# Kernel optimization log

Measured on AMD Instinct MI355X. Metric: run time of the kernel, lower is better.

The kernel has to match this reference:

```python
import jax, jax.numpy as jnp
import numpy as np

H = 4  # num_heads

def _ln(x, g, b):
    m = x.mean(-1, keepdims=True)
    v = ((x - m) ** 2).mean(-1, keepdims=True)
    return (x - m) * jax.lax.rsqrt(v + 1e-5) * g + b

def _mlp(x, w1, b1, w2, b2):
    return jax.nn.relu(x @ w1 + b1) @ w2 + b2

def _lin_att(q, k, v):
    # q,k,v: [BB, L, H, hd] ; linear (kernelized) attention, no softmax
    L = q.shape[1]
    qn = q / jnp.maximum(jnp.linalg.norm(q, axis=-1, keepdims=True), 1e-12)
    kn = k / jnp.maximum(jnp.linalg.norm(k, axis=-1, keepdims=True), 1e-12)
    kvs = jnp.einsum('blhm,blhd->bhmd', kn, v)
    num = jnp.einsum('bnhm,bhmd->bnhd', qn, kvs) + L * v
    den = jnp.einsum('bnhm,bhm->bnh', qn, kn.sum(axis=1))[..., None] + L
    return num / den

def _fast_attn(x4, w_qkv, w_op, b_op):
    # x4: [B,T,N,D]; spatial attention over N, temporal attention over T, concat, project
    B, T, N, D = x4.shape
    hd = D // H
    q, k, v = jnp.split(x4 @ w_qkv, 3, axis=-1)
    sh = lambda t: t.reshape(B * T, N, H, hd)
    out_s = _lin_att(sh(q), sh(k), sh(v)).reshape(B, T, N, D)
    th = lambda t: jnp.swapaxes(t, 1, 2).reshape(B * N, T, H, hd)
    out_t = jnp.swapaxes(_lin_att(th(q), th(k), th(v)).reshape(B, N, T, D), 1, 2)
    return jnp.concatenate([out_s, out_t], axis=-1) @ w_op + b_op

def _forward(x, W_in, b_in, adp, W_tp, b_tp, qkv_w, op_w, op_b, pw_w, pw_b,
             fc_w1, fc_b1, fc_w2, fc_b2, ln1_g, ln1_b, ln2_g, ln2_b,
             ep_w, ep_b, enc_w1, enc_b1, enc_w2, enc_b2, out_w, out_b):
    Nn, T, _ = x.shape
    xt = jnp.swapaxes(x, 0, 1)[None]                 # [1,T,N,in]
    h = xt @ W_in + b_in                             # input_proj -> [1,T,N,24]
    h = jnp.concatenate([h, adp[None]], axis=-1)     # + adaptive emb -> [1,T,N,104]
    h = h @ W_tp + b_tp                              # temporal_proj: 1x1 conv == pointwise linear
    graph = jnp.einsum('tnd,tmd->tnm', adp, adp)     # [T,N,N]
    graph = jax.nn.softmax(jax.nn.relu(graph), axis=-1)  # AvgPool(1,1) is identity
    # GraphPropagate (order=2, eval/no-dropout): [h, graph @ h]
    z1 = jnp.einsum('tni,btid->btnd', graph, h)
    att0 = _fast_attn(h, qkv_w[0], op_w[0], op_b[0])
    att1 = _fast_attn(z1, qkv_w[1], op_w[1], op_b[1])
    # scale = [1, 0.01]; note torch's in-place aliasing makes ln1 input = 2*x_glo
    g = h + att0 * (h @ pw_w[0] + pw_b[0]) + 0.01 * att1 * (att0 @ pw_w[1] + pw_b[1])
    h1 = _ln(2.0 * g, ln1_g, ln1_b)
    h2 = _ln(h1 + _mlp(h1, fc_w1, fc_b1, fc_w2, fc_b2), ln2_g, ln2_b)
    y = jnp.swapaxes(h2, 1, 2).reshape(1, Nn, T * h2.shape[-1]) @ ep_w + ep_b  # encoder_proj
    for i in range(enc_w1.shape[0]):                 # 3 residual MLP blocks
        y = y + _mlp(y, enc_w1[i], enc_b1[i], enc_w2[i], enc_b2[i])
    out = y @ out_w + out_b                          # [1,N,365]
    return out.reshape(Nn, T, 1)

def setup_inputs() -> dict:
    key = jax.random.key(0)
    ks = jax.random.split(key, 24)
    f = lambda i, shape, s=0.05: jax.random.normal(ks[i], shape, dtype=jnp.float32) * s
    D, T, N, IN = 104, 365, 400, 3
    return {
        'x': jax.random.normal(ks[0], (N, T, IN), dtype=jnp.float32),
        'W_in': f(1, (IN, 24)), 'b_in': f(2, (24,)),
        'adp': f(3, (T, N, 80)),
        'W_tp': f(4, (D, D)), 'b_tp': f(5, (D,)),
        'qkv_w': f(6, (2, D, 3 * D)),
        'op_w': f(7, (2, 2 * D, D)), 'op_b': f(8, (2, D)),
        'pw_w': f(9, (2, D, D)), 'pw_b': f(10, (2, D)),
        'fc_w1': f(11, (D, 2 * D)), 'fc_b1': f(12, (2 * D,)),
        'fc_w2': f(13, (2 * D, D)), 'fc_b2': f(14, (D,)),
        'ln1_g': jnp.ones((D,), jnp.float32), 'ln1_b': jnp.zeros((D,), jnp.float32),
        'ln2_g': jnp.ones((D,), jnp.float32), 'ln2_b': jnp.zeros((D,), jnp.float32),
        'ep_w': f(15, (T * D, D), 0.01), 'ep_b': f(16, (D,)),
        'enc_w1': f(17, (3, D, 2 * D)), 'enc_b1': f(18, (3, 2 * D)),
        'enc_w2': f(19, (3, 2 * D, D)), 'enc_b2': f(20, (3, D)),
        'out_w': f(21, (D, T)), 'out_b': f(22, (T,)),
    }

def reference(x, W_in, b_in, adp, W_tp, b_tp, qkv_w, op_w, op_b, pw_w, pw_b,
              fc_w1, fc_b1, fc_w2, fc_b2, ln1_g, ln1_b, ln2_g, ln2_b,
              ep_w, ep_b, enc_w1, enc_b1, enc_w2, enc_b2, out_w, out_b):
    return _forward(x, W_in, b_in, adp, W_tp, b_tp, qkv_w, op_w, op_b, pw_w, pw_b,
                    fc_w1, fc_b1, fc_w2, fc_b2, ln1_g, ln1_b, ln2_g, ln2_b,
                    ep_w, ep_b, enc_w1, enc_b1, enc_w2, enc_b2, out_w, out_b)
```

## Files before the change

### kernel.cpp

```cpp
#include <hip/hip_runtime.h>
#include <hip/hip_bf16.h>
#include <cstddef>

#define TT   365
#define NN   400
#define TN   (TT*NN)
#define HD   26
#define NH   4

#define CEILDIV(a,b) (((a)+(b)-1)/(b))

typedef __hip_bfloat16 bf16;
typedef short short8v __attribute__((ext_vector_type(8)));
typedef float float4v __attribute__((ext_vector_type(4)));
typedef float float16v __attribute__((ext_vector_type(16)));
__device__ __forceinline__ float b2f(bf16 v){ return __bfloat162float(v); }
__device__ __forceinline__ bf16  f2b(float v){ return __float2bfloat16(v); }

static constexpr size_t NB0 = (size_t)TN*104;
static constexpr size_t NB1 = (size_t)TN*104;
static constexpr size_t NB2 = (size_t)TN*312;
static constexpr size_t NB3 = (size_t)TN*104;
static constexpr size_t NBF = NB0+NB1+NB2+NB3;
static constexpr size_t NTILE   = (size_t)108*32;
static constexpr size_t NKVSB_S = (size_t)TT*NTILE;
static constexpr size_t NKVSB_T = (size_t)NN*NTILE;
static constexpr size_t NY      = (size_t)NN*104;
static constexpr size_t NW_TP   = 104*128;
static constexpr size_t NW_QKV  = 312*128;
static constexpr size_t NW_OP   = 104*224;
static constexpr size_t NW_PW   = 104*128;
static constexpr size_t NW_FC1  = 208*128;
static constexpr size_t NW_FC2  = 104*224;
static constexpr size_t NW_EPT  = (size_t)104*37960;
static constexpr size_t NWT     = NW_TP + 2*NW_QKV + 2*NW_OP + 2*NW_PW + NW_FC1 + NW_FC2 + NW_EPT;
static constexpr size_t WS_NEEDED = NBF*2 + (NKVSB_S+NKVSB_T)*2 + NY*4 + NWT*2;
static constexpr size_t NADP_ROWS = (size_t)TN + 64;
static constexpr size_t NADP = NADP_ROWS*96;
static constexpr size_t NHT  = ((size_t)TT*104 + 8)*448;
static_assert(NADP + NHT <= NB2, "z1 scratch must fit in B2");

__global__ void __launch_bounds__(256) prep_w(
    const float* __restrict__ W, bf16* __restrict__ Wt, int K, int Nc, int KP)
{
    int idx = blockIdx.x*256 + threadIdx.x;
    if (idx >= Nc*KP) return;
    int n = idx / KP, k = idx - n*KP;
    Wt[idx] = (k < K) ? f2b(W[(size_t)k*Nc + n]) : f2b(0.f);
}

__global__ void __launch_bounds__(256) prep_wT(
    const float* __restrict__ W, bf16* __restrict__ Wt)
{
    __shared__ float T[64][105];
    int k0 = blockIdx.x * 64;
    int tid = threadIdx.x;
    for (int idx = tid; idx < 64*104; idx += 256) {
        int r = idx / 104, c = idx - r*104;
        int k = k0 + r;
        T[r][c] = (k < 37960) ? W[(size_t)k*104 + c] : 0.f;
    }
    __syncthreads();
    for (int idx = tid; idx < 104*32; idx += 256) {
        int n = idx >> 5, kp = idx & 31;
        int k = kp*2;
        if (k0 + k + 1 < 37960 || k0 + k < 37960) {
            if (k0 + k < 37960) {
                bf16 lo = f2b(T[k][n]);
                bf16 hi = f2b(T[k+1][n]);
                uint v = ((uint)(*(ushort*)&hi) << 16) | (*(ushort*)&lo);
                if (k0 + k + 1 < 37960) *(uint*)(Wt + (size_t)n*37960 + k0 + k) = v;
                else Wt[(size_t)n*37960 + k0 + k] = lo;
            }
        }
    }
}

__global__ void __launch_bounds__(256) prep_adp(
    const float* __restrict__ adp, bf16* __restrict__ out)
{
    size_t i = (size_t)blockIdx.x*256 + threadIdx.x;
    if (i >= NADP) return;
    size_t row = i / 96; int e = (int)(i - row*96);
    float v = (row < TN && e < 80) ? adp[row*80 + e] : 0.f;
    out[i] = f2b(v);
}

__global__ void __launch_bounds__(256) ht_kernel(
    const bf16* __restrict__ h, bf16* __restrict__ hT)
{
    __shared__ bf16 As[64*106];
    int t = blockIdx.y, n0 = blockIdx.x*64;
    int tid = threadIdx.x;
    for (int idx = tid; idx < 64*52; idx += 256) {
        int r = idx / 52, k = idx - r*52;
        int n = n0 + r;
        uint v = 0;
        if (n < NN) v = *(const uint*)(h + ((size_t)t*NN + n)*104 + k*2);
        *(uint*)(&As[r*106 + k*2]) = v;
    }
    __syncthreads();
    for (int idx = tid; idx < 104*32; idx += 256) {
        int d = idx >> 5, np = idx & 31;
        int n = np*2;
        ushort lo = *(ushort*)&As[n*106 + d];
        ushort hi = *(ushort*)&As[(n+1)*106 + d];
        uint v = ((uint)hi << 16) | lo;
        *(uint*)(hT + ((size_t)t*104 + d)*448 + n0 + n) = v;
    }
}

__global__ void __launch_bounds__(128) hcat_kernel(
    const float* __restrict__ x, const float* __restrict__ W_in,
    const float* __restrict__ b_in, const float* __restrict__ adp,
    bf16* __restrict__ hcat)
{
    int bid = blockIdx.x;
    int t = bid / NN, n = bid - t*NN;
    int tid = threadIdx.x;
    if (tid < 24) {
        float s = b_in[tid];
        size_t xb = ((size_t)n*TT + t)*3;
        #pragma unroll
        for (int i = 0; i < 3; ++i) s += x[xb + i] * W_in[i*24 + tid];
        hcat[(size_t)bid*104 + tid] = f2b(s);
    } else if (tid < 104) {
        hcat[(size_t)bid*104 + tid] = f2b(adp[(size_t)bid*80 + (tid - 24)]);
    }
}

template<int KP>
__global__ void __launch_bounds__(256) gemm_mf(
    const bf16* __restrict__ A, int lda, int K,
    const bf16* __restrict__ Wt, const float* __restrict__ bias,
    bf16* __restrict__ C, int M, int Nc, int relu)
{
    constexpr int STR = KP + 8;
    constexpr int KPQ = KP/8;
    __shared__ bf16 As[64*STR];
    __shared__ bf16 Ws[64*STR];
    int m0 = blockIdx.x * 64;
    int c0 = blockIdx.y * 64;
    int tid = threadIdx.x;
    const int KQ = K/8;
    uint4 z4 = {0u,0u,0u,0u};
    for (int idx = tid; idx < 64*KPQ; idx += 256) {
        int r = idx / KPQ, q = idx - r*KPQ;
        int m = m0 + r;
        uint4 v = z4;
        if (m < M && q < KQ) v = *(const uint4*)(A + (size_t)m*lda + q*8);
        *(uint4*)(&As[r*STR + q*8]) = v;
    }
    for (int idx = tid; idx < 64*KPQ; idx += 256) {
        int r = idx / KPQ, q = idx - r*KPQ;
        int n = c0 + r;
        uint4 v = z4;
        if (n < Nc) v = *(const uint4*)(Wt + (size_t)n*KP + q*8);
        *(uint4*)(&Ws[r*STR + q*8]) = v;
    }
    __syncthreads();

    int lane = tid & 63, w = tid >> 6;
    int n16 = lane & 15, quad = lane >> 4;
    constexpr int KS = KP/32;
    short8v af[KS];
    #pragma unroll
    for (int s = 0; s < KS; ++s)
        af[s] = *(const short8v*)(&As[(16*w + n16)*STR + s*32 + quad*8]);
    float4v acc[4];
    #pragma unroll
    for (int ct = 0; ct < 4; ++ct) { float4v z = {0.f,0.f,0.f,0.f}; acc[ct] = z; }
    #pragma unroll
    for (int ct = 0; ct < 4; ++ct) {
        #pragma unroll
        for (int s = 0; s < KS; ++s) {
            short8v bfr = *(const short8v*)(&Ws[(ct*16 + n16)*STR + s*32 + quad*8]);
            acc[ct] = __builtin_amdgcn_mfma_f32_16x16x32_bf16(af[s], bfr, acc[ct], 0, 0, 0);
        }
    }
    #pragma unroll
    for (int ct = 0; ct < 4; ++ct) {
        int c = c0 + ct*16 + n16;
        if (c < Nc) {
            float b = bias ? bias[c] : 0.f;
            #pragma unroll
            for (int reg = 0; reg < 4; ++reg) {
                int m = m0 + 16*w + quad*4 + reg;
                if (m < M) {
                    float v = acc[ct][reg] + b;
                    if (relu) v = fmaxf(v, 0.f);
                    C[(size_t)m*Nc + c] = f2b(v);
                }
            }
        }
    }
}

__global__ void __launch_bounds__(256) gate_ln1(
    bf16* __restrict__ h, const bf16* __restrict__ att0, const bf16* __restrict__ att1,
    const bf16* __restrict__ w0t, const bf16* __restrict__ w1t, const float* __restrict__ pwb,
    const float* __restrict__ gamma, const float* __restrict__ beta)
{
    constexpr int STR = 136;
    __shared__ bf16 A0s[64*STR];
    __shared__ bf16 A1s[64*STR];
    __shared__ bf16 Ws[112*STR];
    __shared__ float prm[416];
    int m0 = blockIdx.x * 64;
    int tid = threadIdx.x;
    int lane = tid & 63, w = tid >> 6, n16 = lane & 15, quad = lane >> 4;
    uint4 z4 = {0u,0u,0u,0u};

    for (int idx = tid; idx < 64*16; idx += 256) {
        int r = idx >> 4, q = idx & 15;
        int m = m0 + r;
        uint4 v0 = z4, v1 = z4;
        if (m < TN && q < 13) {
            v0 = *(const uint4*)(h    + (size_t)m*104 + q*8);
            v1 = *(const uint4*)(att0 + (size_t)m*104 + q*8);
        }
        *(uint4*)(&A0s[r*STR + q*8]) = v0;
        *(uint4*)(&A1s[r*STR + q*8]) = v1;
    }
    for (int idx = tid; idx < 112*16; idx += 256) {
        int c = idx >> 4, q = idx & 15;
        uint4 v = z4;
        if (c < 104) v = *(const uint4*)(w0t + (size_t)c*128 + q*8);
        *(uint4*)(&Ws[c*STR + q*8]) = v;
    }
    for (int i = tid; i < 416; i += 256)
        prm[i] = (i < 208) ? pwb[i] : (i < 312 ? gamma[i-208] : beta[i-312]);
    __syncthreads();

    short8v a0f[4], a1f[4];
    #pragma unroll
    for (int s = 0; s < 4; ++s) {
        a0f[s] = *(const short8v*)(&A0s[(16*w + n16)*STR + s*32 + quad*8]);
        a1f[s] = *(const short8v*)(&A1s[(16*w + n16)*STR + s*32 + quad*8]);
    }
    float4v acc0[7], acc1[7];
    #pragma unroll
    for (int ct = 0; ct < 7; ++ct) { float4v z = {0.f,0.f,0.f,0.f}; acc0[ct] = z; acc1[ct] = z; }
    #pragma unroll
    for (int ct = 0; ct < 7; ++ct)
        #pragma unroll
        for (int s = 0; s < 4; ++s) {
            short8v bfr = *(const short8v*)(&Ws[(ct*16 + n16)*STR + s*32 + quad*8]);
            acc0[ct] = __builtin_amdgcn_mfma_f32_16x16x32_bf16(a0f[s], bfr, acc0[ct], 0, 0, 0);
        }
    __syncthreads();
    for (int idx = tid; idx < 112*16; idx += 256) {
        int c = idx >> 4, q = idx & 15;
        uint4 v = z4;
        if (c < 104) v = *(const uint4*)(w1t + (size_t)c*128 + q*8);
        *(uint4*)(&Ws[c*STR + q*8]) = v;
    }
    __syncthreads();
    #pragma unroll
    for (int ct = 0; ct < 7; ++ct)
        #pragma unroll
        for (int s = 0; s < 4; ++s) {
            short8v bfr = *(const short8v*)(&Ws[(ct*16 + n16)*STR + s*32 + quad*8]);
            acc1[ct] = __builtin_amdgcn_mfma_f32_16x16x32_bf16(a1f[s], bfr, acc1[ct], 0, 0, 0);
        }

    float sum[4] = {0.f,0.f,0.f,0.f};
    #pragma unroll
    for (int ct = 0; ct < 7; ++ct) {
        int c = ct*16 + n16;
        bool colok = c < 104;
        float b0 = colok ? prm[c] : 0.f;
        float b1 = colok ? prm[104 + c] : 0.f;
        #pragma unroll
        for (int reg = 0; reg < 4; ++reg) {
            int r = 16*w + quad*4 + reg;
            int m = m0 + r;
            float xv = 0.f;
            if (colok && m < TN) {
                float p0 = acc0[ct][reg] + b0;
                float p1 = acc1[ct][reg] + b1;
                float hv = b2f(A0s[r*STR + c]);
                float a0 = b2f(A1s[r*STR + c]);
                float a1 = b2f(att1[(size_t)m*104 + c]);
                xv = 2.f*(hv + a0*p0 + 0.01f*a1*p1);
            }
            acc0[ct][reg] = xv;
            sum[reg] += xv;
        }
    }
    #pragma unroll
    for (int reg = 0; reg < 4; ++reg) {
        float v = sum[reg];
        v += __shfl_xor(v,1,64); v += __shfl_xor(v,2,64);
        v += __shfl_xor(v,4,64); v += __shfl_xor(v,8,64);
        sum[reg] = v * (1.f/104.f);
    }
    float var[4] = {0.f,0.f,0.f,0.f};
    #pragma unroll
    for (int ct = 0; ct < 7; ++ct) {
        bool colok = (ct*16 + n16) < 104;
        #pragma unroll
        for (int reg = 0; reg < 4; ++reg) {
            if (colok) {
                float d = acc0[ct][reg] - sum[reg];
                acc0[ct][reg] = d;
                var[reg] += d*d;
            }
        }
    }
    #pragma unroll
    for (int reg = 0; reg < 4; ++reg) {
        float v = var[reg];
        v += __shfl_xor(v,1,64); v += __shfl_xor(v,2,64);
        v += __shfl_xor(v,4,64); v += __shfl_xor(v,8,64);
        var[reg] = rsqrtf(v * (1.f/104.f) + 1e-5f);
    }
    #pragma unroll
    for (int ct = 0; ct < 7; ++ct) {
        int c = ct*16 + n16;
        if (c < 104) {
            float g = prm[208 + c], be = prm[312 + c];
            #pragma unroll
            for (int reg = 0; reg < 4; ++reg) {
                int m = m0 + 16*w + quad*4 + reg;
                if (m < TN)
                    h[(size_t)m*104 + c] = f2b(acc0[ct][reg]*var[reg]*g + be);
            }
        }
    }
}

__global__ void __launch_bounds__(256) fc2_ln2(
    const bf16* __restrict__ hidden, const bf16* __restrict__ w2t, const float* __restrict__ b2,
    const bf16* __restrict__ h1, const float* __restrict__ gamma, const float* __restrict__ beta,
    bf16* __restrict__ h2)
{
    constexpr int STRA = 232;
    constexpr int STRW = 136;
    __shared__ bf16 As[64*STRA];
    __shared__ bf16 Ws[112*STRW];
    __shared__ float prm[312];
    int m0 = blockIdx.x * 64;
    int tid = threadIdx.x;
    int lane = tid & 63, w = tid >> 6, n16 = lane & 15, quad = lane >> 4;
    uint4 z4 = {0u,0u,0u,0u};

    for (int idx = tid; idx < 64*28; idx += 256) {
        int r = idx / 28, q = idx - r*28;
        int m = m0 + r;
        uint4 v = z4;
        if (m < TN && q < 26) v = *(const uint4*)(hidden + (size_t)m*208 + q*8);
        *(uint4*)(&As[r*STRA + q*8]) = v;
    }
    for (int idx = tid; idx < 112*16; idx += 256) {
        int c = idx >> 4, q = idx & 15;
        uint4 v = z4;
        if (c < 104) v = *(const uint4*)(w2t + (size_t)c*224 + q*8);
        *(uint4*)(&Ws[c*STRW + q*8]) = v;
    }
    for (int i = tid; i < 312; i += 256)
        prm[i] = (i < 104) ? b2[i] : (i < 208 ? gamma[i-104] : beta[i-208]);
    __syncthreads();

    short8v af[7];
    #pragma unroll
    for (int s = 0; s < 7; ++s)
        af[s] = *(const short8v*)(&As[(16*w + n16)*STRA + s*32 + quad*8]);
    float4v acc[7];
    #pragma unroll
    for (int ct = 0; ct < 7; ++ct) { float4v z = {0.f,0.f,0.f,0.f}; acc[ct] = z; }
    #pragma unroll
    for (int ct = 0; ct < 7; ++ct)
        #pragma unroll
        for (int s = 0; s < 4; ++s) {
            short8v bfr = *(const short8v*)(&Ws[(ct*16 + n16)*STRW + s*32 + quad*8]);
            acc[ct] = __builtin_amdgcn_mfma_f32_16x16x32_bf16(af[s], bfr, acc[ct], 0, 0, 0);
        }
    __syncthreads();
    for (int idx = tid; idx < 112*16; idx += 256) {
        int c = idx >> 4, q = idx & 15;
        uint4 v = z4;
        if (c < 104 && q < 12) v = *(const uint4*)(w2t + (size_t)c*224 + 128 + q*8);
        *(uint4*)(&Ws[c*STRW + q*8]) = v;
    }
    __syncthreads();
    #pragma unroll
    for (int ct = 0; ct < 7; ++ct)
        #pragma unroll
        for (int s = 4; s < 7; ++s) {
            short8v bfr = *(const short8v*)(&Ws[(ct*16 + n16)*STRW + (s-4)*32 + quad*8]);
            acc[ct] = __builtin_amdgcn_mfma_f32_16x16x32_bf16(af[s], bfr, acc[ct], 0, 0, 0);
        }

    float sum[4] = {0.f,0.f,0.f,0.f};
    #pragma unroll
    for (int ct = 0; ct < 7; ++ct) {
        int c = ct*16 + n16;
        bool colok = c < 104;
        float bb = colok ? prm[c] : 0.f;
        #pragma unroll
        for (int reg = 0; reg < 4; ++reg) {
            int m = m0 + 16*w + quad*4 + reg;
            float xv = 0.f;
            if (colok && m < TN)
                xv = b2f(h1[(size_t)m*104 + c]) + acc[ct][reg] + bb;
            acc[ct][reg] = xv;
            sum[reg] += xv;
        }
    }
    #pragma unroll
    for (int reg = 0; reg < 4; ++reg) {
        float v = sum[reg];
        v += __shfl_xor(v,1,64); v += __shfl_xor(v,2,64);
        v += __shfl_xor(v,4,64); v += __shfl_xor(v,8,64);
        sum[reg] = v * (1.f/104.f);
    }
    float var[4] = {0.f,0.f,0.f,0.f};
    #pragma unroll
    for (int ct = 0; ct < 7; ++ct) {
        bool colok = (ct*16 + n16) < 104;
        #pragma unroll
        for (int reg = 0; reg < 4; ++reg) {
            if (colok) {
                float d = acc[ct][reg] - sum[reg];
                acc[ct][reg] = d;
                var[reg] += d*d;
            }
        }
    }
    #pragma unroll
    for (int reg = 0; reg < 4; ++reg) {
        float v = var[reg];
        v += __shfl_xor(v,1,64); v += __shfl_xor(v,2,64);
        v += __shfl_xor(v,4,64); v += __shfl_xor(v,8,64);
        var[reg] = rsqrtf(v * (1.f/104.f) + 1e-5f);
    }
    #pragma unroll
    for (int ct = 0; ct < 7; ++ct) {
        int c = ct*16 + n16;
        if (c < 104) {
            float g = prm[104 + c], be = prm[208 + c];
            #pragma unroll
            for (int reg = 0; reg < 4; ++reg) {
                int m = m0 + 16*w + quad*4 + reg;
                if (m < TN)
                    h2[(size_t)m*104 + c] = f2b(acc[ct][reg]*var[reg]*g + be);
            }
        }
    }
}

__global__ void __launch_bounds__(256) ep_mf(
    const bf16* __restrict__ h2, const bf16* __restrict__ wt, float* __restrict__ y)
{
    constexpr int STR = 136;
    __shared__ bf16 As[64*STR];
    __shared__ bf16 Ws[64*STR];
    int m0 = blockIdx.x * 64;
    int c0 = blockIdx.y * 64;
    int t0 = blockIdx.z * 8;
    int t1 = min(TT, t0 + 8);
    int tid = threadIdx.x;
    int lane = tid & 63, w = tid >> 6, n16 = lane & 15, quad = lane >> 4;
    uint4 z4 = {0u,0u,0u,0u};

    float4v acc[4];
    #pragma unroll
    for (int ct = 0; ct < 4; ++ct) { float4v z = {0.f,0.f,0.f,0.f}; acc[ct] = z; }

    for (int t = t0; t < t1; ++t) {
        for (int idx = tid; idx < 64*16; idx += 256) {
            int r = idx >> 4, q = idx & 15;
            int m = m0 + r;
            uint4 va = z4;
            if (m < NN && q < 13) va = *(const uint4*)(h2 + ((size_t)t*NN + m)*104 + q*8);
            *(uint4*)(&As[r*STR + q*8]) = va;
            int c = c0 + r;
            uint4 vw = z4;
            if (c < 104 && q < 13) vw = *(const uint4*)(wt + (size_t)c*37960 + t*104 + q*8);
            *(uint4*)(&Ws[r*STR + q*8]) = vw;
        }
        __syncthreads();
        short8v af[4];
        #pragma unroll
        for (int s = 0; s < 4; ++s)
            af[s] = *(const short8v*)(&As[(16*w + n16)*STR + s*32 + quad*8]);
        #pragma unroll
        for (int ct = 0; ct < 4; ++ct) {
            #pragma unroll
            for (int s = 0; s < 4; ++s) {
                short8v bfr = *(const short8v*)(&Ws[(ct*16 + n16)*STR + s*32 + quad*8]);
                acc[ct] = __builtin_amdgcn_mfma_f32_16x16x32_bf16(af[s], bfr, acc[ct], 0, 0, 0);
            }
        }
        __syncthreads();
    }
    #pragma unroll
    for (int ct = 0; ct < 4; ++ct) {
        int c = c0 + ct*16 + n16;
        if (c < 104) {
            #pragma unroll
            for (int reg = 0; reg < 4; ++reg) {
                int m = m0 + 16*w + quad*4 + reg;
                if (m < NN) atomicAdd(&y[(size_t)m*104 + c], acc[ct][reg]);
            }
        }
    }
}

static constexpr int Z1_TQ = CEILDIV(TT, 8);
static constexpr int Z1_BLOCKS = 8 * Z1_TQ * 7;
__global__ void __launch_bounds__(256, 4) z1_mf(
    const bf16* __restrict__ adp_bf, const bf16* __restrict__ hT, bf16* __restrict__ z1)
{
    constexpr int SA = 104;
    constexpr int SP = 72;
    __shared__ bf16 Bt[64*SA];
    __shared__ bf16 Hs[104*SP];
    __shared__ bf16 P[64*SP];
    bf16* As = Hs;

    int bid = blockIdx.x;
    int xcd = bid & 7;
    int j = bid >> 3;
    int tq = j / 7, rblk = j - tq*7;
    int t = tq*8 + xcd;
    if (t >= TT) return;
    int r0 = rblk*64;

    int tid = threadIdx.x;
    int lane = tid & 63, w = tid >> 6, n16 = lane & 15, quad = lane >> 4;

    {
        const uint4* src = (const uint4*)(adp_bf + ((size_t)t*NN + r0)*96);
        for (int idx = tid; idx < 768; idx += 256) {
            int r = idx / 12, q = idx - r*12;
            *(uint4*)(&As[r*SA + q*8]) = src[idx];
        }
    }
    __syncthreads();
    short8v af[3];
    #pragma unroll
    for (int s = 0; s < 3; ++s)
        af[s] = *(const short8v*)(&As[(16*w + n16)*SA + s*32 + quad*8]);
    __syncthreads();

    float4v onum[7];
    #pragma unroll
    for (int dt = 0; dt < 7; ++dt) { float4v z = {0.f,0.f,0.f,0.f}; onum[dt] = z; }
    float rs[4] = {0.f,0.f,0.f,0.f};

    uint4 preB[3], preH[4];
    {
        const uint4* srcB = (const uint4*)(adp_bf + (size_t)t*NN*96);
        #pragma unroll
        for (int j2 = 0; j2 < 3; ++j2) preB[j2] = srcB[tid + j2*256];
        const bf16* hb = hT + (size_t)t*104*448;
        #pragma unroll
        for (int j2 = 0; j2 < 4; ++j2) {
            int idx = tid + j2*256;
            uint4 v = {0u,0u,0u,0u};
            if (idx < 832) {
                int d = idx >> 3, q = idx & 7;
                v = *(const uint4*)(hb + (size_t)d*448 + q*8);
            }
            preH[j2] = v;
        }
    }

    for (int c0 = 0; c0 < NN; c0 += 64) {
        #pragma unroll
        for (int j2 = 0; j2 < 3; ++j2) {
            int idx = tid + j2*256;
            int r = idx / 12, q = idx - r*12;
            *(uint4*)(&Bt[r*SA + q*8]) = preB[j2];
        }
        #pragma unroll
        for (int j2 = 0; j2 < 4; ++j2) {
            int idx = tid + j2*256;
            if (idx < 832) {
                int d = idx >> 3, q = idx & 7;
                *(uint4*)(&Hs[d*SP + q*8]) = preH[j2];
            }
        }
        __syncthreads();
        int cn = c0 + 64;
        if (cn < NN) {
            const uint4* srcB = (const uint4*)(adp_bf + ((size_t)t*NN + cn)*96);
            #pragma unroll
            for (int j2 = 0; j2 < 3; ++j2) preB[j2] = srcB[tid + j2*256];
            const bf16* hb = hT + (size_t)t*104*448 + cn;
            #pragma unroll
            for (int j2 = 0; j2 < 4; ++j2) {
                int idx = tid + j2*256;
                if (idx < 832) {
                    int d = idx >> 3, q = idx & 7;
                    preH[j2] = *(const uint4*)(hb + (size_t)d*448 + q*8);
                }
            }
        }
        float4v sc[4];
        #pragma unroll
        for (int ct = 0; ct < 4; ++ct) { float4v z = {0.f,0.f,0.f,0.f}; sc[ct] = z; }
        #pragma unroll
        for (int ct = 0; ct < 4; ++ct) {
            #pragma unroll
            for (int s = 0; s < 3; ++s) {
                short8v bfr = *(const short8v*)(&Bt[(ct*16 + n16)*SA + s*32 + quad*8]);
                sc[ct] = __builtin_amdgcn_mfma_f32_16x16x32_bf16(af[s], bfr, sc[ct], 0, 0, 0);
            }
        }
        #pragma unroll
        for (int ct = 0; ct < 4; ++ct) {
            bool colok = (c0 + ct*16 + n16) < NN;
            #pragma unroll
            for (int reg = 0; reg < 4; ++reg) {
                float e = colok ? __expf(fmaxf(sc[ct][reg], 0.f)) : 0.f;
                rs[reg] += e;
                P[(16*w + quad*4 + reg)*SP + ct*16 + n16] = f2b(e);
            }
        }
        short8v pf[2];
        #pragma unroll
        for (int s = 0; s < 2; ++s)
            pf[s] = *(const short8v*)(&P[(16*w + n16)*SP + s*32 + quad*8]);
        #pragma unroll
        for (int dt = 0; dt < 7; ++dt) {
            int hr = dt*16 + n16;
            if (hr > 103) hr = 103;
            #pragma unroll
            for (int s = 0; s < 2; ++s) {
                short8v bfr = *(const short8v*)(&Hs[hr*SP + s*32 + quad*8]);
                onum[dt] = __builtin_amdgcn_mfma_f32_16x16x32_bf16(pf[s], bfr, onum[dt], 0, 0, 0);
            }
        }
        __syncthreads();
    }
    #pragma unroll
    for (int reg = 0; reg < 4; ++reg) {
        float v = rs[reg];
        v += __shfl_xor(v, 1, 64);
        v += __shfl_xor(v, 2, 64);
        v += __shfl_xor(v, 4, 64);
        v += __shfl_xor(v, 8, 64);
        rs[reg] = v;
    }
    #pragma unroll
    for (int reg = 0; reg < 4; ++reg) {
        int row = r0 + 16*w + quad*4 + reg;
        if (row < NN) {
            float inv = 1.f / rs[reg];
            #pragma unroll
            for (int dt = 0; dt < 7; ++dt) {
                int d = dt*16 + n16;
                if (d < 104)
                    z1[((size_t)t*NN + row)*104 + d] = f2b(onum[dt][reg] * inv);
            }
        }
    }
}

__global__ void __launch_bounds__(256) kvs_mf(
    const bf16* __restrict__ qkv, bf16* __restrict__ kvsb_s, bf16* __restrict__ kvsb_t)
{
    constexpr int CK = 32;
    constexpr int TS = 40;
    __shared__ bf16 raw[CK][216];
    __shared__ bf16 kTn[4][32][TS];
    __shared__ bf16 vT [4][32][TS];
    __shared__ float invs[CK][4];

    int bb = blockIdx.x;
    bf16* out; int L; long long strideL, base;
    if (bb < TT) { out = kvsb_s + (size_t)bb*NTILE; L = NN; base = (long long)bb*NN*312 + 104; strideL = 312; }
    else { int n = bb - TT; out = kvsb_t + (size_t)n*NTILE; L = TT; base = (long long)n*312 + 104; strideL = (long long)NN*312; }

    int tid = threadIdx.x;
    int lane = tid & 63, w = tid >> 6;
    int n32 = lane & 31, koct = lane >> 5;
    uint4 z4 = {0u,0u,0u,0u};

    float16v acc;
    #pragma unroll
    for (int i = 0; i < 16; ++i) acc[i] = 0.f;

    uint4 pre[4];
    #pragma unroll
    for (int j = 0; j < 4; ++j) {
        int idx = tid + j*256;
        uint4 v = z4;
        if (idx < CK*26) {
            int r = idx / 26, q = idx - r*26;
            if (r < L) v = *(const uint4*)(qkv + base + (long long)r*strideL + q*8);
        }
        pre[j] = v;
    }

    for (int l0 = 0; l0 < L; l0 += CK) {
        int lw = min(CK, L - l0);
        __syncthreads();
        #pragma unroll
        for (int j = 0; j < 4; ++j) {
            int idx = tid + j*256;
            if (idx < CK*26) {
                int r = idx / 26, q = idx - r*26;
                *(uint4*)(&raw[r][q*8]) = pre[j];
            }
        }
        __syncthreads();
        {
            int ln0 = l0 + CK;
            #pragma unroll
            for (int j = 0; j < 4; ++j) {
                int idx = tid + j*256;
                uint4 v = z4;
                if (idx < CK*26 && ln0 < L) {
                    int r = idx / 26, q = idx - r*26;
                    if (r < L - ln0) v = *(const uint4*)(qkv + base + (long long)(ln0 + r)*strideL + q*8);
                }
                pre[j] = v;
            }
        }
        if (tid < CK*4) {
            int l = tid >> 2, h = tid & 3;
            float ss = 0.f;
            #pragma unroll
            for (int m = 0; m < HD; ++m) { float v = b2f(raw[l][h*HD + m]); ss += v*v; }
            invs[l][h] = (l < lw) ? 1.f/fmaxf(sqrtf(ss), 1e-12f) : 0.f;
        }
        __syncthreads();
        for (int idx = tid; idx < 4*CK*HD; idx += 256) {
            int h = idx / (CK*HD); int rem = idx - h*CK*HD;
            int l = rem / HD; int m = rem - l*HD;
            float iv = invs[l][h];
            kTn[h][m][l] = f2b(b2f(raw[l][h*HD + m]) * iv);
            vT[h][m][l]  = raw[l][104 + h*HD + m];
        }
        if (tid < 4*CK) {
            int h = tid >> 5, l = tid & 31;
            vT[h][26][l] = f2b((l < lw) ? 1.f : 0.f);
        }
        __syncthreads();
        #pragma unroll
        for (int s = 0; s < 2; ++s) {
            short8v a = *(const short8v*)(&kTn[w][n32][s*16 + koct*8]);
            short8v b = *(const short8v*)(&vT [w][n32][s*16 + koct*8]);
            acc = __builtin_amdgcn_mfma_f32_32x32x16_bf16(a, b, acc, 0, 0, 0);
        }
    }

    int lo = w*HD;
    #pragma unroll
    for (int reg = 0; reg < 16; ++reg) {
        int m = (reg & 3) + 8*(reg >> 2) + 4*koct;
        if (m < HD) {
            if (n32 < HD)       out[(size_t)(lo + n32)*32 + m] = f2b(acc[reg]);
            else if (n32 == HD) out[(size_t)(104 + w)*32 + m] = f2b(acc[reg]);
        }
    }
}

__global__ void __launch_bounds__(256) attn_mm(
    bf16* __restrict__ qkv, const bf16* __restrict__ kvsb,
    int M, long long bStride, long long rowStride, float Lf, int outOff)
{
    constexpr int STR = 136;
    __shared__ bf16 As[64*STR];
    __shared__ bf16 Ws[112*STR];
    __shared__ float nsqL[64*4];
    __shared__ float denL[64*4];
    int mt = blockIdx.x, bb = blockIdx.y;
    int tid = threadIdx.x;
    int lane = tid & 63, w = tid >> 6, n16 = lane & 15, quad = lane >> 4;
    bf16* base = qkv + (size_t)bb * bStride;
    int r0 = mt*64;
    uint4 z4 = {0u,0u,0u,0u};

    for (int idx = tid; idx < 64*16; idx += 256) {
        int r = idx >> 4, q = idx & 15;
        int m = r0 + r;
        uint4 v = z4;
        if (m < M && q < 13) v = *(const uint4*)(base + (size_t)m*rowStride + q*8);
        *(uint4*)(&As[r*STR + q*8]) = v;
    }
    for (int idx = tid; idx < 112*16; idx += 256) {
        int c = idx >> 4, q = idx & 15;
        *(uint4*)(&Ws[c*STR + q*8]) = z4;
    }
    __syncthreads();
    {
        const bf16* kb = kvsb + (size_t)bb * NTILE;
        for (int idx = tid; idx < 108*13; idx += 256) {
            int c = idx / 13, qu = idx - c*13;
            int lo = (c < 104) ? (c/26)*26 : (c-104)*26;
            *(uint*)(&Ws[c*STR + lo + qu*2]) = *(const uint*)(kb + (size_t)c*32 + qu*2);
        }
    }
    __syncthreads();

    short8v af[4];
    #pragma unroll
    for (int s = 0; s < 4; ++s)
        af[s] = *(const short8v*)(&As[(16*w + n16)*STR + s*32 + quad*8]);
    float4v acc[7];
    #pragma unroll
    for (int ct = 0; ct < 7; ++ct) { float4v z = {0.f,0.f,0.f,0.f}; acc[ct] = z; }
    #pragma unroll
    for (int ct = 0; ct < 7; ++ct) {
        #pragma unroll
        for (int s = 0; s < 4; ++s) {
            short8v bfr = *(const short8v*)(&Ws[(ct*16 + n16)*STR + s*32 + quad*8]);
            acc[ct] = __builtin_amdgcn_mfma_f32_16x16x32_bf16(af[s], bfr, acc[ct], 0, 0, 0);
        }
    }
    {
        int row = tid >> 2, hh = tid & 3;
        const bf16* qr = &As[row*STR + hh*26];
        float ss = 0.f;
        #pragma unroll
        for (int m = 0; m < HD; ++m) { float v = b2f(qr[m]); ss += v*v; }
        nsqL[row*4 + hh] = ss;
    }
    if (n16 >= 8 && n16 < 12) {
        #pragma unroll
        for (int reg = 0; reg < 4; ++reg)
            denL[(16*w + quad*4 + reg)*4 + (n16 - 8)] = acc[6][reg];
    }
    __syncthreads();
    #pragma unroll
    for (int ct = 0; ct < 7; ++ct) {
        int c = ct*16 + n16;
        if (c < 104) {
            int hh = c / 26;
            #pragma unroll
            for (int reg = 0; reg < 4; ++reg) {
                int lr = 16*w + quad*4 + reg;
                int m = r0 + lr;
                if (m < M) {
                    float iq = 1.f / fmaxf(sqrtf(nsqL[lr*4 + hh]), 1e-12f);
                    float den = iq * denL[lr*4 + hh] + Lf;
                    bf16* rp = base + (size_t)m*rowStride;
                    float num = iq * acc[ct][reg] + Lf * b2f(rp[208 + c]);
                    rp[outOff + c] = f2b(num / den);
                }
            }
        }
    }
}

__global__ void __launch_bounds__(256) y_init_kernel(float* __restrict__ y, const float* __restrict__ ep_b) {
    int i = blockIdx.x*256 + threadIdx.x;
    if (i < NN*104) y[i] = ep_b[i % 104];
}

__global__ void __launch_bounds__(256) enc_kernel(
    float* __restrict__ y, const float* __restrict__ w1, const float* __restrict__ b1,
    const float* __restrict__ w2, const float* __restrict__ b2)
{
    int n = blockIdx.x;
    int tid = threadIdx.x;
    __shared__ float yr[104], hid[208];
    if (tid < 104) yr[tid] = y[(size_t)n*104 + tid];
    __syncthreads();
    if (tid < 208) {
        float s = b1[tid];
        for (int k = 0; k < 104; ++k) s += yr[k] * w1[(size_t)k*208 + tid];
        hid[tid] = fmaxf(s, 0.f);
    }
    __syncthreads();
    if (tid < 104) {
        float s = b2[tid];
        for (int k = 0; k < 208; ++k) s += hid[k] * w2[(size_t)k*104 + tid];
        y[(size_t)n*104 + tid] = yr[tid] + s;
    }
}

__global__ void __launch_bounds__(256) out_kernel(
    const float* __restrict__ y, const float* __restrict__ out_w,
    const float* __restrict__ out_b, float* __restrict__ out)
{
    int n = blockIdx.x;
    int tid = threadIdx.x;
    __shared__ float yr[104];
    if (tid < 104) yr[tid] = y[(size_t)n*104 + tid];
    __syncthreads();
    for (int t = tid; t < TT; t += 256) {
        float s = out_b[t];
        for (int d = 0; d < 104; ++d) s += yr[d] * out_w[(size_t)d*TT + t];
        out[(size_t)n*TT + t] = s;
    }
}

extern "C" void kernel_launch(void* const* d_in, const int* in_sizes, int n_in,
                              void* d_out, int out_size, void* d_ws, size_t ws_size,
                              hipStream_t stream) {
    if (ws_size < WS_NEEDED) return;

    const float* x      = (const float*)d_in[0];
    const float* W_in   = (const float*)d_in[1];
    const float* b_in   = (const float*)d_in[2];
    const float* adp    = (const float*)d_in[3];
    const float* W_tp   = (const float*)d_in[4];
    const float* b_tp   = (const float*)d_in[5];
    const float* qkv_w  = (const float*)d_in[6];
    const float* op_w   = (const float*)d_in[7];
    const float* op_b   = (const float*)d_in[8];
    const float* pw_w   = (const float*)d_in[9];
    const float* pw_b   = (const float*)d_in[10];
    const float* fc_w1  = (const float*)d_in[11];
    const float* fc_b1  = (const float*)d_in[12];
    const float* fc_w2  = (const float*)d_in[13];
    const float* fc_b2  = (const float*)d_in[14];
    const float* ln1_g  = (const float*)d_in[15];
    const float* ln1_b  = (const float*)d_in[16];
    const float* ln2_g  = (const float*)d_in[17];
    const float* ln2_b  = (const float*)d_in[18];
    const float* ep_w   = (const float*)d_in[19];
    const float* ep_b   = (const float*)d_in[20];
    const float* enc_w1 = (const float*)d_in[21];
    const float* enc_b1 = (const float*)d_in[22];
    const float* enc_w2 = (const float*)d_in[23];
    const float* enc_b2 = (const float*)d_in[24];
    const float* out_w  = (const float*)d_in[25];
    const float* out_b  = (const float*)d_in[26];

    bf16* B0 = (bf16*)d_ws;
    bf16* B1 = B0 + NB0;
    bf16* B2 = B1 + NB1;
    bf16* B3 = B2 + NB2;
    bf16* kvsb_s = B3 + NB3;
    bf16* kvsb_t = kvsb_s + NKVSB_S;
    float* ybuf  = (float*)(kvsb_t + NKVSB_T);
    bf16* wtp   = (bf16*)(ybuf + NY);
    bf16* wqkv0 = wtp + NW_TP;
    bf16* wqkv1 = wqkv0 + NW_QKV;
    bf16* wop0  = wqkv1 + NW_QKV;
    bf16* wop1  = wop0 + NW_OP;
    bf16* wpw0  = wop1 + NW_OP;
    bf16* wpw1  = wpw0 + NW_PW;
    bf16* wfc1  = wpw1 + NW_PW;
    bf16* wfc2  = wfc1 + NW_FC1;
    bf16* wept  = wfc2 + NW_FC2;
    bf16* adp_bf = B2;
    bf16* hTbuf  = B2 + NADP;

    prep_w<<<CEILDIV(104*128,256), 256, 0, stream>>>(W_tp, wtp, 104, 104, 128);
    prep_w<<<CEILDIV(312*128,256), 256, 0, stream>>>(qkv_w, wqkv0, 104, 312, 128);
    prep_w<<<CEILDIV(312*128,256), 256, 0, stream>>>(qkv_w + 104*312, wqkv1, 104, 312, 128);
    prep_w<<<CEILDIV(104*224,256), 256, 0, stream>>>(op_w, wop0, 208, 104, 224);
    prep_w<<<CEILDIV(104*224,256), 256, 0, stream>>>(op_w + 208*104, wop1, 208, 104, 224);
    prep_w<<<CEILDIV(104*128,256), 256, 0, stream>>>(pw_w, wpw0, 104, 104, 128);
    prep_w<<<CEILDIV(104*128,256), 256, 0, stream>>>(pw_w + 104*104, wpw1, 104, 104, 128);
    prep_w<<<CEILDIV(208*128,256), 256, 0, stream>>>(fc_w1, wfc1, 104, 208, 128);
    prep_w<<<CEILDIV(104*224,256), 256, 0, stream>>>(fc_w2, wfc2, 208, 104, 224);
    prep_wT<<<CEILDIV(37960,64), 256, 0, stream>>>(ep_w, wept);

    const int GX = CEILDIV(TN, 64);
    dim3 g4(GX, 4), g5(GX, 5);

    hcat_kernel<<<TN, 128, 0, stream>>>(x, W_in, b_in, adp, B2);
    gemm_mf<128><<<dim3(GX,2), 256, 0, stream>>>(B2, 104, 104, wtp, b_tp, B0, TN, 104, 0);
    prep_adp<<<CEILDIV((int)NADP,256), 256, 0, stream>>>(adp, adp_bf);
    ht_kernel<<<dim3(7, TT), 256, 0, stream>>>(B0, hTbuf);
    z1_mf<<<Z1_BLOCKS, 256, 0, stream>>>(adp_bf, hTbuf, B1);
    gemm_mf<128><<<g5, 256, 0, stream>>>(B0, 104, 104, wqkv0, nullptr, B2, TN, 312, 0);
    kvs_mf<<<TT+NN, 256, 0, stream>>>(B2, kvsb_s, kvsb_t);
    attn_mm<<<dim3(6, NN), 256, 0, stream>>>(B2, kvsb_t, TT, 312, (long long)NN*312, (float)TT, 104);
    attn_mm<<<dim3(7, TT), 256, 0, stream>>>(B2, kvsb_s, NN, (long long)NN*312, 312, (float)NN, 0);
    gemm_mf<224><<<dim3(GX,2), 256, 0, stream>>>(B2, 312, 208, wop0, op_b, B3, TN, 104, 0);
    gemm_mf<128><<<g5, 256, 0, stream>>>(B1, 104, 104, wqkv1, nullptr, B2, TN, 312, 0);
    kvs_mf<<<TT+NN, 256, 0, stream>>>(B2, kvsb_s, kvsb_t);
    attn_mm<<<dim3(6, NN), 256, 0, stream>>>(B2, kvsb_t, TT, 312, (long long)NN*312, (float)TT, 104);
    attn_mm<<<dim3(7, TT), 256, 0, stream>>>(B2, kvsb_s, NN, (long long)NN*312, 312, (float)NN, 0);
    gemm_mf<224><<<dim3(GX,2), 256, 0, stream>>>(B2, 312, 208, wop1, op_b + 104, B1, TN, 104, 0);
    gate_ln1<<<GX, 256, 0, stream>>>(B0, B3, B1, wpw0, wpw1, pw_b, ln1_g, ln1_b);
    gemm_mf<128><<<g4, 256, 0, stream>>>(B0, 104, 104, wfc1, fc_b1, B2, TN, 208, 1);
    fc2_ln2<<<GX, 256, 0, stream>>>(B2, wfc2, fc_b2, B0, ln2_g, ln2_b, B3);
    y_init_kernel<<<CEILDIV(NN*104,256), 256, 0, stream>>>(ybuf, ep_b);
    ep_mf<<<dim3(CEILDIV(NN,64), 2, CEILDIV(TT,8)), 256, 0, stream>>>(B3, wept, ybuf);
    for (int i = 0; i < 3; ++i)
        enc_kernel<<<NN, 256, 0, stream>>>(ybuf, enc_w1 + (size_t)i*104*208, enc_b1 + (size_t)i*208,
                                           enc_w2 + (size_t)i*208*104, enc_b2 + (size_t)i*104);
    out_kernel<<<NN, 256, 0, stream>>>(ybuf, out_w, out_b, (float*)d_out);
}
```

Before: 1.339 ms.

## Remap GEMM blocks per XCD and move z1 kernel to 32x32 MFMA tiles

The GEMM launches become 1D grids that remap block IDs so that consecutive tiles sharing the same A rows land on the same XCD, aiming for better L2 reuse of A across column tiles. The z1 graph-propagation kernel switches from 16x16x32 to 32x32x16 MFMA, with each wave owning a 32x32 quadrant of scores. The 64-row row sums are reduced through shared memory, and the H tile is padded to 128 rows with zeroed padding. The larger tiles cut LDS fragment reads per MFMA, at the cost of more accumulator registers, an extra barrier per chunk and a lower occupancy hint (3 instead of 4).

```diff
diff --git a/kernel.cpp b/kernel.cpp
--- a/kernel.cpp
+++ b/kernel.cpp
@@ -139,8 +139,15 @@
     constexpr int KPQ = KP/8;
     __shared__ bf16 As[64*STR];
     __shared__ bf16 Ws[64*STR];
-    int m0 = blockIdx.x * 64;
-    int c0 = blockIdx.y * 64;
+    int nCol = (Nc + 63) >> 6;
+    int nwg = gridDim.x;
+    int bid = blockIdx.x;
+    int xcd = bid & 7, kk = bid >> 3;
+    int q8 = nwg >> 3, r8 = nwg & 7;
+    int widx = (xcd < r8 ? xcd*(q8+1) : r8*(q8+1) + (xcd - r8)*q8) + kk;
+    int mblk = widx / nCol;
+    int m0 = mblk * 64;
+    int c0 = (widx - mblk*nCol) * 64;
     int tid = threadIdx.x;
     const int KQ = K/8;
     uint4 z4 = {0u,0u,0u,0u};
@@ -510,14 +517,16 @@
 
 static constexpr int Z1_TQ = CEILDIV(TT, 8);
 static constexpr int Z1_BLOCKS = 8 * Z1_TQ * 7;
-__global__ void __launch_bounds__(256, 4) z1_mf(
+__global__ void __launch_bounds__(256, 3) z1_mf(
     const bf16* __restrict__ adp_bf, const bf16* __restrict__ hT, bf16* __restrict__ z1)
 {
-    constexpr int SA = 104;
-    constexpr int SP = 72;
+    constexpr int SA  = 104;
+    constexpr int SPH = 72;
+    constexpr int SPP = 72;
     __shared__ bf16 Bt[64*SA];
-    __shared__ bf16 Hs[104*SP];
-    __shared__ bf16 P[64*SP];
+    __shared__ bf16 Hs[128*SPH];
+    __shared__ bf16 P [64*SPP];
+    __shared__ float rsb[2][64];
     bf16* As = Hs;
 
     int bid = blockIdx.x;
@@ -529,7 +538,9 @@
     int r0 = rblk*64;
 
     int tid = threadIdx.x;
-    int lane = tid & 63, w = tid >> 6, n16 = lane & 15, quad = lane >> 4;
+    int lane = tid & 63, w = tid >> 6;
+    int n32 = lane & 31, koct = lane >> 5;
+    int qi = w >> 1, ci = w & 1;
 
     {
         const uint4* src = (const uint4*)(adp_bf + ((size_t)t*NN + r0)*96);
@@ -539,16 +550,25 @@
         }
     }
     __syncthreads();
-    short8v af[3];
-    #pragma unroll
-    for (int s = 0; s < 3; ++s)
-        af[s] = *(const short8v*)(&As[(16*w + n16)*SA + s*32 + quad*8]);
-    __syncthreads();
-
-    float4v onum[7];
-    #pragma unroll
-    for (int dt = 0; dt < 7; ++dt) { float4v z = {0.f,0.f,0.f,0.f}; onum[dt] = z; }
-    float rs[4] = {0.f,0.f,0.f,0.f};
+    short8v af2[6];
+    #pragma unroll
+    for (int s = 0; s < 6; ++s)
+        af2[s] = *(const short8v*)(&As[(qi*32 + n32)*SA + s*16 + koct*8]);
+    __syncthreads();
+    {
+        uint4 z4v = {0u,0u,0u,0u};
+        for (int idx = tid; idx < 216; idx += 256) {
+            int r = 104 + idx/9, q = idx - (idx/9)*9;
+            *(uint4*)(&Hs[r*SPH + q*8]) = z4v;
+        }
+    }
+
+    float16v onum0, onum1;
+    #pragma unroll
+    for (int i = 0; i < 16; ++i) { onum0[i] = 0.f; onum1[i] = 0.f; }
+    float rs2[16];
+    #pragma unroll
+    for (int i = 0; i < 16; ++i) rs2[i] = 0.f;
 
     uint4 preB[3], preH[4];
     {
@@ -580,7 +600,7 @@
             int idx = tid + j2*256;
             if (idx < 832) {
                 int d = idx >> 3, q = idx & 7;
-                *(uint4*)(&Hs[d*SP + q*8]) = preH[j2];
+                *(uint4*)(&Hs[d*SPH + q*8]) = preH[j2];
             }
         }
         __syncthreads();
@@ -599,63 +619,69 @@
                 }
             }
         }
-        float4v sc[4];
-        #pragma unroll
-        for (int ct = 0; ct < 4; ++ct) { float4v z = {0.f,0.f,0.f,0.f}; sc[ct] = z; }
-        #pragma unroll
-        for (int ct = 0; ct < 4; ++ct) {
-            #pragma unroll
-            for (int s = 0; s < 3; ++s) {
-                short8v bfr = *(const short8v*)(&Bt[(ct*16 + n16)*SA + s*32 + quad*8]);
-                sc[ct] = __builtin_amdgcn_mfma_f32_16x16x32_bf16(af[s], bfr, sc[ct], 0, 0, 0);
-            }
-        }
-        #pragma unroll
-        for (int ct = 0; ct < 4; ++ct) {
-            bool colok = (c0 + ct*16 + n16) < NN;
-            #pragma unroll
-            for (int reg = 0; reg < 4; ++reg) {
-                float e = colok ? __expf(fmaxf(sc[ct][reg], 0.f)) : 0.f;
-                rs[reg] += e;
-                P[(16*w + quad*4 + reg)*SP + ct*16 + n16] = f2b(e);
-            }
-        }
-        short8v pf[2];
-        #pragma unroll
-        for (int s = 0; s < 2; ++s)
-            pf[s] = *(const short8v*)(&P[(16*w + n16)*SP + s*32 + quad*8]);
-        #pragma unroll
-        for (int dt = 0; dt < 7; ++dt) {
-            int hr = dt*16 + n16;
-            if (hr > 103) hr = 103;
-            #pragma unroll
-            for (int s = 0; s < 2; ++s) {
-                short8v bfr = *(const short8v*)(&Hs[hr*SP + s*32 + quad*8]);
-                onum[dt] = __builtin_amdgcn_mfma_f32_16x16x32_bf16(pf[s], bfr, onum[dt], 0, 0, 0);
-            }
+        float16v sc;
+        #pragma unroll
+        for (int i = 0; i < 16; ++i) sc[i] = 0.f;
+        #pragma unroll
+        for (int s = 0; s < 6; ++s) {
+            short8v bfr = *(const short8v*)(&Bt[(ci*32 + n32)*SA + s*16 + koct*8]);
+            sc = __builtin_amdgcn_mfma_f32_32x32x16_bf16(af2[s], bfr, sc, 0, 0, 0);
+        }
+        bool colok = (c0 + ci*32 + n32) < NN;
+        #pragma unroll
+        for (int reg = 0; reg < 16; ++reg) {
+            int crow = (reg & 3) + 8*(reg >> 2) + 4*koct;
+            float e = colok ? __expf(fmaxf(sc[reg], 0.f)) : 0.f;
+            rs2[reg] += e;
+            P[(qi*32 + crow)*SPP + ci*32 + n32] = f2b(e);
         }
         __syncthreads();
-    }
-    #pragma unroll
-    for (int reg = 0; reg < 4; ++reg) {
-        float v = rs[reg];
+        short8v pA[4];
+        #pragma unroll
+        for (int s = 0; s < 4; ++s)
+            pA[s] = *(const short8v*)(&P[(qi*32 + n32)*SPP + s*16 + koct*8]);
+        int dt0 = (w & 1), dt1 = dt0 + 2;
+        #pragma unroll
+        for (int s = 0; s < 4; ++s) {
+            short8v hb0 = *(const short8v*)(&Hs[(dt0*32 + n32)*SPH + s*16 + koct*8]);
+            onum0 = __builtin_amdgcn_mfma_f32_32x32x16_bf16(pA[s], hb0, onum0, 0, 0, 0);
+        }
+        #pragma unroll
+        for (int s = 0; s < 4; ++s) {
+            short8v hb1 = *(const short8v*)(&Hs[(dt1*32 + n32)*SPH + s*16 + koct*8]);
+            onum1 = __builtin_amdgcn_mfma_f32_32x32x16_bf16(pA[s], hb1, onum1, 0, 0, 0);
+        }
+        __syncthreads();
+    }
+
+    #pragma unroll
+    for (int reg = 0; reg < 16; ++reg) {
+        float v = rs2[reg];
         v += __shfl_xor(v, 1, 64);
         v += __shfl_xor(v, 2, 64);
         v += __shfl_xor(v, 4, 64);
         v += __shfl_xor(v, 8, 64);
-        rs[reg] = v;
-    }
-    #pragma unroll
-    for (int reg = 0; reg < 4; ++reg) {
-        int row = r0 + 16*w + quad*4 + reg;
-        if (row < NN) {
-            float inv = 1.f / rs[reg];
-            #pragma unroll
-            for (int dt = 0; dt < 7; ++dt) {
-                int d = dt*16 + n16;
-                if (d < 104)
-                    z1[((size_t)t*NN + row)*104 + d] = f2b(onum[dt][reg] * inv);
-            }
+        v += __shfl_xor(v, 16, 64);
+        if (n32 == 0) {
+            int crow = (reg & 3) + 8*(reg >> 2) + 4*koct;
+            rsb[ci][qi*32 + crow] = v;
+        }
+    }
+    __syncthreads();
+
+    int dt0 = (w & 1), dt1 = dt0 + 2;
+    #pragma unroll
+    for (int reg = 0; reg < 16; ++reg) {
+        int crow = (reg & 3) + 8*(reg >> 2) + 4*koct;
+        int qrow = qi*32 + crow;
+        int gq = r0 + qrow;
+        if (gq < NN) {
+            float inv = 1.f / (rsb[0][qrow] + rsb[1][qrow]);
+            int d0 = dt0*32 + n32;
+            z1[((size_t)t*NN + gq)*104 + d0] = f2b(onum0[reg] * inv);
+            int d1 = dt1*32 + n32;
+            if (d1 < 104)
+                z1[((size_t)t*NN + gq)*104 + d1] = f2b(onum1[reg] * inv);
         }
     }
 }
@@ -956,25 +982,24 @@
     prep_wT<<<CEILDIV(37960,64), 256, 0, stream>>>(ep_w, wept);
 
     const int GX = CEILDIV(TN, 64);
-    dim3 g4(GX, 4), g5(GX, 5);
 
     hcat_kernel<<<TN, 128, 0, stream>>>(x, W_in, b_in, adp, B2);
-    gemm_mf<128><<<dim3(GX,2), 256, 0, stream>>>(B2, 104, 104, wtp, b_tp, B0, TN, 104, 0);
+    gemm_mf<128><<<GX*2, 256, 0, stream>>>(B2, 104, 104, wtp, b_tp, B0, TN, 104, 0);
     prep_adp<<<CEILDIV((int)NADP,256), 256, 0, stream>>>(adp, adp_bf);
     ht_kernel<<<dim3(7, TT), 256, 0, stream>>>(B0, hTbuf);
     z1_mf<<<Z1_BLOCKS, 256, 0, stream>>>(adp_bf, hTbuf, B1);
-    gemm_mf<128><<<g5, 256, 0, stream>>>(B0, 104, 104, wqkv0, nullptr, B2, TN, 312, 0);
+    gemm_mf<128><<<GX*5, 256, 0, stream>>>(B0, 104, 104, wqkv0, nullptr, B2, TN, 312, 0);
     kvs_mf<<<TT+NN, 256, 0, stream>>>(B2, kvsb_s, kvsb_t);
     attn_mm<<<dim3(6, NN), 256, 0, stream>>>(B2, kvsb_t, TT, 312, (long long)NN*312, (float)TT, 104);
     attn_mm<<<dim3(7, TT), 256, 0, stream>>>(B2, kvsb_s, NN, (long long)NN*312, 312, (float)NN, 0);
-    gemm_mf<224><<<dim3(GX,2), 256, 0, stream>>>(B2, 312, 208, wop0, op_b, B3, TN, 104, 0);
-    gemm_mf<128><<<g5, 256, 0, stream>>>(B1, 104, 104, wqkv1, nullptr, B2, TN, 312, 0);
+    gemm_mf<224><<<GX*2, 256, 0, stream>>>(B2, 312, 208, wop0, op_b, B3, TN, 104, 0);
+    gemm_mf<128><<<GX*5, 256, 0, stream>>>(B1, 104, 104, wqkv1, nullptr, B2, TN, 312, 0);
     kvs_mf<<<TT+NN, 256, 0, stream>>>(B2, kvsb_s, kvsb_t);
     attn_mm<<<dim3(6, NN), 256, 0, stream>>>(B2, kvsb_t, TT, 312, (long long)NN*312, (float)TT, 104);
     attn_mm<<<dim3(7, TT), 256, 0, stream>>>(B2, kvsb_s, NN, (long long)NN*312, 312, (float)NN, 0);
-    gemm_mf<224><<<dim3(GX,2), 256, 0, stream>>>(B2, 312, 208, wop1, op_b + 104, B1, TN, 104, 0);
+    gemm_mf<224><<<GX*2, 256, 0, stream>>>(B2, 312, 208, wop1, op_b + 104, B1, TN, 104, 0);
     gate_ln1<<<GX, 256, 0, stream>>>(B0, B3, B1, wpw0, wpw1, pw_b, ln1_g, ln1_b);
-    gemm_mf<128><<<g4, 256, 0, stream>>>(B0, 104, 104, wfc1, fc_b1, B2, TN, 208, 1);
+    gemm_mf<128><<<GX*4, 256, 0, stream>>>(B0, 104, 104, wfc1, fc_b1, B2, TN, 208, 1);
     fc2_ln2<<<GX, 256, 0, stream>>>(B2, wfc2, fc_b2, B0, ln2_g, ln2_b, B3);
     y_init_kernel<<<CEILDIV(NN*104,256), 256, 0, stream>>>(ybuf, ep_b);
     ep_mf<<<dim3(CEILDIV(NN,64), 2, CEILDIV(TT,8)), 256, 0, stream>>>(B3, wept, ybuf);
```

Result: no change. 1.320 ms (-1.4%).
